# Performance work log

Measured on AMD Instinct MI355X. Metric: run time of the kernel, lower is better.

Reference implementation:

```python
import jax, jax.numpy as jnp
import numpy as np

B, L, DIN = 16, 4096, 1280
DM, N, R, NL = 128, 16, 8, 2  # d_model=d_inner, d_state, dt_rank, num_layers


def setup_inputs() -> dict:
    key = jax.random.key(0)
    ks = jax.random.split(key, 16)
    f = lambda i, shape, s=0.02: jax.random.normal(ks[i], shape, jnp.float32) * s
    return dict(
        x=jax.random.normal(ks[0], (B, L, DIN), jnp.float32),
        ip_w=f(1, (DM, DIN)), ip_b=f(2, (DM,)),
        in_w=f(3, (NL, 2 * DM, DM)),              # in_proj (no bias), out = [x; z]
        conv_w=f(4, (NL, DM, 2), 0.5), conv_b=f(5, (NL, DM)),  # depthwise causal conv, k=2
        xp_w=f(6, (NL, R + 2 * N, DM)),           # x_proj -> [dt; B; C]
        dt_w=f(7, (NL, DM, R), 0.5), dt_b=f(8, (NL, DM)),
        A_log=jnp.broadcast_to(jnp.log(jnp.arange(1, N + 1, dtype=jnp.float32)), (NL, DM, N)),
        Dp=jnp.ones((NL, DM), jnp.float32),
        out_w=f(9, (NL, DM, DM)),
        ln_g=jnp.ones((DM,), jnp.float32), ln_b=jnp.zeros((DM,), jnp.float32),
        c1_w=f(10, (64, DM)), c1_b=f(11, (64,)),
        c2_w=f(12, (2, 64)), c2_b=f(13, (2,)),
    )


def _mamba(x, in_w, conv_w, conv_b, xp_w, dt_w, dt_b, A_log, Dp, out_w):
    # x: [B,L,DM]
    Bsz, Ls, _ = x.shape
    xz = jnp.einsum('bld,ed->ble', x, in_w)          # [B,L,2*DM]
    u, z = jnp.split(xz, 2, axis=-1)                  # each [B,L,DM]
    # causal depthwise conv, kernel size 2: y_t = w0*u_{t-1} + w1*u_t + b
    u_prev = jnp.pad(u, ((0, 0), (1, 0), (0, 0)))[:, :Ls]
    u = jax.nn.silu(u_prev * conv_w[:, 0] + u * conv_w[:, 1] + conv_b)
    proj = jnp.einsum('bld,ed->ble', u, xp_w)         # [B,L,R+2N]
    dt, Bm, Cm = jnp.split(proj, [R, R + N], axis=-1)
    delta = jax.nn.softplus(jnp.einsum('blr,dr->bld', dt, dt_w) + dt_b)  # [B,L,DM]
    A = -jnp.exp(A_log)                               # [DM,N]

    def step(h, inp):
        d_t, b_t, c_t, u_t = inp                      # [B,DM],[B,N],[B,N],[B,DM]
        dA = jnp.exp(d_t[..., None] * A)              # [B,DM,N]
        h = h * dA + (d_t * u_t)[..., None] * b_t[:, None, :]
        y = jnp.einsum('bdn,bn->bd', h, c_t)
        return h, y

    h0 = jnp.zeros((Bsz, DM, N), x.dtype)
    xs = (delta.transpose(1, 0, 2), Bm.transpose(1, 0, 2),
          Cm.transpose(1, 0, 2), u.transpose(1, 0, 2))
    _, ys = jax.lax.scan(step, h0, xs)                # ys: [L,B,DM]
    y = ys.transpose(1, 0, 2) + u * Dp
    y = y * jax.nn.silu(z)
    return jnp.einsum('bld,ed->ble', y, out_w)


def reference(x, ip_w, ip_b, in_w, conv_w, conv_b, xp_w, dt_w, dt_b, A_log, Dp,
              out_w, ln_g, ln_b, c1_w, c1_b, c2_w, c2_b):
    h = jnp.einsum('bli,di->bld', x, ip_w) + ip_b     # input_proj
    for l in range(NL):                               # residual Mamba blocks
        h = h + _mamba(h, in_w[l], conv_w[l], conv_b[l], xp_w[l], dt_w[l],
                       dt_b[l], A_log[l], Dp[l], out_w[l])
    mu = jnp.mean(h, -1, keepdims=True)
    var = jnp.mean((h - mu) ** 2, -1, keepdims=True)
    h = (h - mu) / jnp.sqrt(var + 1e-5) * ln_g + ln_b # LayerNorm
    p = jnp.mean(h, axis=1)                           # mean pool over seq
    p = jax.nn.relu(p @ c1_w.T + c1_b)                # classifier (dropout=eval/no-op)
    return p @ c2_w.T + c2_b                          # [B,2]
```

## Files before the change

### kernel.cpp

```cpp
#include <hip/hip_runtime.h>
#include <hip/hip_bf16.h>
#include <cstdint>

#define B_   16
#define L_   4096
#define DIN_ 1280
#define DM_  128
#define NS_  16
#define RR_  8
#define NL_  2
#define M_   (B_ * L_)
#define NC_  128
#define CL_  (L_ / NC_)

typedef short short8 __attribute__((ext_vector_type(8)));
typedef float f32x4  __attribute__((ext_vector_type(4)));
typedef unsigned short ushort;
typedef ushort ushort4v __attribute__((ext_vector_type(4)));

__device__ __forceinline__ float silu_f(float x) { return x / (1.f + __expf(-x)); }

__device__ __forceinline__ ushort f2bf(float f) {
  union { float f; uint32_t u; } v; v.f = f;
  uint32_t u = v.u;
  u += 0x7fffu + ((u >> 16) & 1u);
  return (ushort)(u >> 16);
}

#define LDK 40

__global__ __launch_bounds__(256) void gemm_mfma(
    const float* __restrict__ A, const float* __restrict__ W,
    const float* __restrict__ bias,
    float* __restrict__ C0, float* __restrict__ C1,
    int M, int Nc, int K, int split, int residual)
{
  __shared__ ushort As[128 * LDK];
  __shared__ ushort Ws[128 * LDK];
  const int tid = threadIdx.x;
  const int n0 = blockIdx.x * 128;
  const int m0 = blockIdx.y * 128;

  const int srow = tid >> 1;
  const int scol = (tid & 1) << 4;
  const float* gA = A + (size_t)(m0 + srow) * K + scol;
  const float* gW = W + (size_t)(n0 + srow) * K + scol;

  const int lane = tid & 63;
  const int wv = tid >> 6;
  const int wm = (wv & 1) * 64, wn = (wv >> 1) * 64;
  const int ln15 = lane & 15, quad = lane >> 4;

  f32x4 acc[4][4];
#pragma unroll
  for (int i = 0; i < 4; ++i)
#pragma unroll
    for (int j = 0; j < 4; ++j) acc[i][j] = (f32x4){0.f, 0.f, 0.f, 0.f};

  float4 fa[4], fw[4];
#pragma unroll
  for (int j = 0; j < 4; ++j) {
    fa[j] = *(const float4*)(gA + j * 4);
    fw[j] = *(const float4*)(gW + j * 4);
  }

  for (int k0 = 0; k0 < K; k0 += 32) {
    __syncthreads();
#pragma unroll
    for (int j = 0; j < 4; ++j) {
      ushort4v a4 = { f2bf(fa[j].x), f2bf(fa[j].y), f2bf(fa[j].z), f2bf(fa[j].w) };
      ushort4v w4 = { f2bf(fw[j].x), f2bf(fw[j].y), f2bf(fw[j].z), f2bf(fw[j].w) };
      *(ushort4v*)&As[srow * LDK + scol + j * 4] = a4;
      *(ushort4v*)&Ws[srow * LDK + scol + j * 4] = w4;
    }
    if (k0 + 32 < K) {
#pragma unroll
      for (int j = 0; j < 4; ++j) {
        fa[j] = *(const float4*)(gA + k0 + 32 + j * 4);
        fw[j] = *(const float4*)(gW + k0 + 32 + j * 4);
      }
    }
    __syncthreads();
    short8 aF[4], bF[4];
#pragma unroll
    for (int mt = 0; mt < 4; ++mt)
      aF[mt] = *(const short8*)&As[(wm + mt * 16 + ln15) * LDK + quad * 8];
#pragma unroll
    for (int nt = 0; nt < 4; ++nt)
      bF[nt] = *(const short8*)&Ws[(wn + nt * 16 + ln15) * LDK + quad * 8];
#pragma unroll
    for (int mt = 0; mt < 4; ++mt)
#pragma unroll
      for (int nt = 0; nt < 4; ++nt)
        acc[mt][nt] = __builtin_amdgcn_mfma_f32_16x16x32_bf16(
            aF[mt], bF[nt], acc[mt][nt], 0, 0, 0);
  }

  const bool left = n0 < split;
#pragma unroll
  for (int mt = 0; mt < 4; ++mt) {
    const int row = m0 + wm + mt * 16 + quad * 4;
#pragma unroll
    for (int nt = 0; nt < 4; ++nt) {
      const int col = n0 + wn + nt * 16 + ln15;
      const float bv = bias ? bias[col] : 0.f;
#pragma unroll
      for (int r = 0; r < 4; ++r) {
        float v = acc[mt][nt][r] + bv;
        if (left) {
          float* p = C0 + (size_t)(row + r) * split + col;
          if (residual) v += *p;
          *p = v;
        } else {
          C1[(size_t)(row + r) * (Nc - split) + (col - split)] = silu_f(v);
        }
      }
    }
  }
}

__global__ __launch_bounds__(256) void xpc(
    const float* __restrict__ uraw,
    const float* __restrict__ cw, const float* __restrict__ cb,
    const float* __restrict__ xpw,
    const float* __restrict__ dtw,
    const float* __restrict__ dtb,
    float* __restrict__ uout,
    float* __restrict__ delta,
    float* __restrict__ BCout)
{
  __shared__ float u_s[32][132];
  __shared__ float xp_s[40 * 128];
  __shared__ float dtw_s[128 * 8];
  __shared__ float dtb_s[128];
  __shared__ float proj_s[32][41];
  const int tid = threadIdx.x;
  const size_t m0 = (size_t)blockIdx.x * 32;
  const int t0 = (int)(m0 & (L_ - 1));

#pragma unroll
  for (int i = 0; i < 16; ++i) {
    int f = tid + i * 256;
    int tok = f >> 7, dd = f & 127;
    float cur = uraw[(m0 + tok) * DM_ + dd];
    float prev = (t0 + tok > 0) ? uraw[(m0 + tok - 1) * DM_ + dd] : 0.f;
    float v = silu_f(cw[dd * 2] * prev + cw[dd * 2 + 1] * cur + cb[dd]);
    u_s[tok][dd] = v;
    uout[(m0 + tok) * DM_ + dd] = v;
  }
  for (int f = tid; f < 40 * 128; f += 256) xp_s[f] = xpw[f];
  for (int f = tid; f < 128 * 8; f += 256) dtw_s[f] = dtw[f];
  if (tid < 128) dtb_s[tid] = dtb[tid];
  __syncthreads();

  {
    const int tok = tid & 31, eg = tid >> 5;
    float pa[5] = {0.f, 0.f, 0.f, 0.f, 0.f};
    for (int dd = 0; dd < 128; dd += 4) {
      float4 uu = *(const float4*)&u_s[tok][dd];
#pragma unroll
      for (int i = 0; i < 5; ++i) {
        float4 xv = *(const float4*)&xp_s[(eg * 5 + i) * 128 + dd];
        pa[i] += uu.x * xv.x + uu.y * xv.y + uu.z * xv.z + uu.w * xv.w;
      }
    }
#pragma unroll
    for (int i = 0; i < 5; ++i) proj_s[tok][eg * 5 + i] = pa[i];
  }
  __syncthreads();

#pragma unroll
  for (int i = 0; i < 4; ++i) {
    int f = tid + i * 256;
    BCout[m0 * 32 + f] = proj_s[f >> 5][8 + (f & 31)];
  }

  {
    const int tok = tid & 31, dg = tid >> 5;
    float pr[8];
#pragma unroll
    for (int r = 0; r < 8; ++r) pr[r] = proj_s[tok][r];
#pragma unroll
    for (int jj = 0; jj < 16; ++jj) {
      int dd = dg * 16 + jj;
      float acc = dtb_s[dd];
#pragma unroll
      for (int r = 0; r < 8; ++r) acc += pr[r] * dtw_s[dd * 8 + r];
      float sp = (acc > 20.f) ? acc : log1pf(__expf(acc));
      u_s[tok][dd] = sp;
    }
  }
  __syncthreads();
#pragma unroll
  for (int i = 0; i < 16; ++i) {
    int f = tid + i * 256;
    delta[(m0 + (f >> 7)) * DM_ + (f & 127)] = u_s[f >> 7][f & 127];
  }
}

__global__ __launch_bounds__(128) void scan_h(
    const float* __restrict__ delta, const float* __restrict__ u,
    const float* __restrict__ BC, const float* __restrict__ alog,
    float* __restrict__ hend, float* __restrict__ Ssum)
{
  const int d = threadIdx.x;
  const int chunk = blockIdx.x, b = blockIdx.y;
  float a[NS_], h[NS_];
#pragma unroll
  for (int n = 0; n < NS_; ++n) {
    a[n] = -__expf(alog[d * NS_ + n]);
    h[n] = 0.f;
  }
  float S = 0.f;
  const size_t rowbase = (size_t)b * L_ + (size_t)chunk * CL_;
  float dlt = delta[rowbase * DM_ + d];
  float uu  = u[rowbase * DM_ + d];
  for (int s = 0; s < CL_; ++s) {
    const float* Brow = BC + (rowbase + s) * 32;
    float Bv[NS_];
#pragma unroll
    for (int n = 0; n < NS_; ++n) Bv[n] = Brow[n];
    float dn = 0.f, un = 0.f;
    if (s + 1 < CL_) {
      dn = delta[(rowbase + s + 1) * DM_ + d];
      un = u[(rowbase + s + 1) * DM_ + d];
    }
    const float du = dlt * uu;
    S += dlt;
#pragma unroll
    for (int n = 0; n < NS_; ++n) {
      float dA = __expf(dlt * a[n]);
      h[n] = fmaf(h[n], dA, du * Bv[n]);
    }
    dlt = dn; uu = un;
  }
  const size_t o = ((size_t)b * NC_ + chunk) * DM_ + d;
  float4* hp = (float4*)(hend + o * NS_);
#pragma unroll
  for (int q = 0; q < 4; ++q)
    hp[q] = make_float4(h[q * 4], h[q * 4 + 1], h[q * 4 + 2], h[q * 4 + 3]);
  Ssum[o] = S;
}

__global__ __launch_bounds__(256) void scan_comb(
    const float* __restrict__ hend, const float* __restrict__ Ssum,
    const float* __restrict__ alog, float* __restrict__ hstart)
{
  const int idx = blockIdx.x * 256 + threadIdx.x;
  const int n = idx & 15;
  const int d = (idx >> 4) & 127;
  const int b = idx >> 11;
  const float a = -__expf(alog[d * NS_ + n]);
  float hs = 0.f;
  for (int c = 0; c < NC_; ++c) {
    const size_t o = ((size_t)b * NC_ + c) * DM_ + d;
    hstart[o * NS_ + n] = hs;
    hs = hend[o * NS_ + n] + __expf(a * Ssum[o]) * hs;
  }
}

__global__ __launch_bounds__(128) void scan_y(
    const float* __restrict__ delta, const float* __restrict__ u,
    const float* __restrict__ zbuf, const float* __restrict__ BC,
    const float* __restrict__ alog, const float* __restrict__ Dpv,
    const float* __restrict__ hstart, float* __restrict__ y)
{
  const int d = threadIdx.x;
  const int chunk = blockIdx.x, b = blockIdx.y;
  float a[NS_], h[NS_];
  const size_t o = ((size_t)b * NC_ + chunk) * DM_ + d;
  const float4* hp = (const float4*)(hstart + o * NS_);
#pragma unroll
  for (int q = 0; q < 4; ++q) {
    float4 v = hp[q];
    h[q * 4] = v.x; h[q * 4 + 1] = v.y; h[q * 4 + 2] = v.z; h[q * 4 + 3] = v.w;
  }
#pragma unroll
  for (int n = 0; n < NS_; ++n) a[n] = -__expf(alog[d * NS_ + n]);
  const float Dd = Dpv[d];
  const size_t rowbase = (size_t)b * L_ + (size_t)chunk * CL_;
  float dlt = delta[rowbase * DM_ + d];
  float uu  = u[rowbase * DM_ + d];
  float zz  = zbuf[rowbase * DM_ + d];
  for (int s = 0; s < CL_; ++s) {
    const float* Brow = BC + (rowbase + s) * 32;
    float Bv[NS_], Cv[NS_];
#pragma unroll
    for (int n = 0; n < NS_; ++n) { Bv[n] = Brow[n]; Cv[n] = Brow[16 + n]; }
    float dn = 0.f, un = 0.f, zn = 0.f;
    if (s + 1 < CL_) {
      dn = delta[(rowbase + s + 1) * DM_ + d];
      un = u[(rowbase + s + 1) * DM_ + d];
      zn = zbuf[(rowbase + s + 1) * DM_ + d];
    }
    const float du = dlt * uu;
    float yv = uu * Dd;
#pragma unroll
    for (int n = 0; n < NS_; ++n) {
      float dA = __expf(dlt * a[n]);
      h[n] = fmaf(h[n], dA, du * Bv[n]);
      yv = fmaf(h[n], Cv[n], yv);
    }
    y[(rowbase + s) * DM_ + d] = yv * zz;
    dlt = dn; uu = un; zz = zn;
  }
}

__global__ __launch_bounds__(256) void lnpool1(
    const float* __restrict__ h, float* __restrict__ partial)
{
  const int b = blockIdx.y, ch = blockIdx.x;
  const int tid = threadIdx.x, wave = tid >> 6, lane = tid & 63;
  float a0 = 0.f, a1 = 0.f;
  const int tbase = ch * 256 + wave * 64;
  for (int i = 0; i < 64; ++i) {
    const float* row = h + ((size_t)b * L_ + tbase + i) * DM_;
    float x0 = row[lane], x1 = row[lane + 64];
    float s = x0 + x1, sq = x0 * x0 + x1 * x1;
    for (int off = 32; off; off >>= 1) { s += __shfl_xor(s, off); sq += __shfl_xor(sq, off); }
    float mu = s * (1.f / 128.f);
    float var = sq * (1.f / 128.f) - mu * mu;
    float rstd = rsqrtf(var + 1e-5f);
    a0 += (x0 - mu) * rstd;
    a1 += (x1 - mu) * rstd;
  }
  __shared__ float ps[4][128];
  ps[wave][lane] = a0;
  ps[wave][lane + 64] = a1;
  __syncthreads();
  if (tid < 128)
    partial[((size_t)b * 16 + ch) * DM_ + tid] = ps[0][tid] + ps[1][tid] + ps[2][tid] + ps[3][tid];
}

__global__ __launch_bounds__(256) void headk(
    const float* __restrict__ partial,
    const float* __restrict__ lng, const float* __restrict__ lnb,
    const float* __restrict__ c1w, const float* __restrict__ c1b,
    const float* __restrict__ c2w, const float* __restrict__ c2b,
    float* __restrict__ out)
{
  __shared__ float pool[16][128];
  __shared__ float p1[16][64];
  const int tid = threadIdx.x;
  for (int i = tid; i < 16 * 128; i += 256) {
    int b = i >> 7, dd = i & 127;
    float s = 0.f;
    for (int c = 0; c < 16; ++c) s += partial[((size_t)b * 16 + c) * DM_ + dd];
    pool[b][dd] = s * (1.f / (float)L_) * lng[dd] + lnb[dd];
  }
  __syncthreads();
  for (int i = tid; i < 16 * 64; i += 256) {
    int b = i >> 6, j = i & 63;
    float acc = c1b[j];
    for (int dd = 0; dd < 128; ++dd) acc += pool[b][dd] * c1w[j * 128 + dd];
    p1[b][j] = fmaxf(acc, 0.f);
  }
  __syncthreads();
  if (tid < 32) {
    int b = tid >> 1, k = tid & 1;
    float acc = c2b[k];
    for (int j = 0; j < 64; ++j) acc += p1[b][j] * c2w[k * 64 + j];
    out[b * 2 + k] = acc;
  }
}

extern "C" void kernel_launch(void* const* d_in, const int* in_sizes, int n_in,
                              void* d_out, int out_size, void* d_ws, size_t ws_size,
                              hipStream_t stream)
{
  (void)in_sizes; (void)n_in; (void)out_size; (void)ws_size;
  const float* x    = (const float*)d_in[0];
  const float* ipw  = (const float*)d_in[1];
  const float* ipb  = (const float*)d_in[2];
  const float* inw  = (const float*)d_in[3];
  const float* cw   = (const float*)d_in[4];
  const float* cb   = (const float*)d_in[5];
  const float* xpw  = (const float*)d_in[6];
  const float* dtw  = (const float*)d_in[7];
  const float* dtb  = (const float*)d_in[8];
  const float* alog = (const float*)d_in[9];
  const float* Dpv  = (const float*)d_in[10];
  const float* outw = (const float*)d_in[11];
  const float* lng  = (const float*)d_in[12];
  const float* lnb  = (const float*)d_in[13];
  const float* c1w  = (const float*)d_in[14];
  const float* c1b  = (const float*)d_in[15];
  const float* c2w  = (const float*)d_in[16];
  const float* c2b  = (const float*)d_in[17];

  float* ws = (float*)d_ws;
  const size_t SZ = (size_t)M_ * DM_;
  float* h      = ws;
  float* yraw   = h + SZ;
  float* zbuf   = yraw + SZ;
  float* ubuf   = zbuf + SZ;
  float* dbuf   = ubuf + SZ;
  float* bc     = dbuf + SZ;
  float* hend   = bc + (size_t)M_ * 32;
  float* hstart = hend + (size_t)B_ * NC_ * DM_ * NS_;
  float* Ssum   = hstart + (size_t)B_ * NC_ * DM_ * NS_;
  float* part   = Ssum + (size_t)B_ * NC_ * DM_;

  gemm_mfma<<<dim3(1, M_ / 128), 256, 0, stream>>>(
      x, ipw, ipb, h, nullptr, M_, DM_, DIN_, DM_, 0);

  for (int l = 0; l < NL_; ++l) {
    gemm_mfma<<<dim3(2, M_ / 128), 256, 0, stream>>>(
        h, inw + (size_t)l * 256 * DM_, nullptr, yraw, zbuf, M_, 256, DM_, DM_, 0);
    xpc<<<M_ / 32, 256, 0, stream>>>(
        yraw, cw + l * DM_ * 2, cb + l * DM_,
        xpw + l * 40 * DM_, dtw + l * DM_ * RR_, dtb + l * DM_,
        ubuf, dbuf, bc);
    scan_h<<<dim3(NC_, B_), 128, 0, stream>>>(
        dbuf, ubuf, bc, alog + l * DM_ * NS_, hend, Ssum);
    scan_comb<<<(B_ * DM_ * NS_) / 256, 256, 0, stream>>>(
        hend, Ssum, alog + l * DM_ * NS_, hstart);
    scan_y<<<dim3(NC_, B_), 128, 0, stream>>>(
        dbuf, ubuf, zbuf, bc, alog + l * DM_ * NS_, Dpv + l * DM_, hstart, yraw);
    gemm_mfma<<<dim3(1, M_ / 128), 256, 0, stream>>>(
        yraw, outw + (size_t)l * DM_ * DM_, nullptr, h, nullptr, M_, DM_, DM_, DM_, 1);
  }

  lnpool1<<<dim3(16, B_), 256, 0, stream>>>(h, part);
  headk<<<1, 256, 0, stream>>>(part, lng, lnb, c1w, c1b, c2w, c2b, (float*)d_out);
}
```

Baseline: 914.1 us.

## Store intermediate activations in bf16 and stage BC rows in shared memory

Intermediate buffers (u, z, delta, B/C projections, y) now hold bf16 instead of fp32, and weights are converted to bf16 once by a small kernel so the GEMMs load half the bytes. The scan kernels stage each chunk's B/C rows into shared memory once rather than re-reading them from global memory at every step, and the chunk-combine loop prefetches the next chunk's values. The aim is to cut memory traffic across the whole pipeline. The cost is lower precision in the delta and state inputs to the recurrence, plus three extra conversion launches per call.

```diff
diff --git a/kernel.cpp b/kernel.cpp
--- a/kernel.cpp
+++ b/kernel.cpp
@@ -17,6 +17,7 @@
 typedef float f32x4  __attribute__((ext_vector_type(4)));
 typedef unsigned short ushort;
 typedef ushort ushort4v __attribute__((ext_vector_type(4)));
+typedef ushort ushort8v __attribute__((ext_vector_type(8)));
 
 __device__ __forceinline__ float silu_f(float x) { return x / (1.f + __expf(-x)); }
 
@@ -26,25 +27,40 @@
   u += 0x7fffu + ((u >> 16) & 1u);
   return (ushort)(u >> 16);
 }
+__device__ __forceinline__ float bf2f(ushort h) {
+  union { uint32_t u; float f; } v; v.u = ((uint32_t)h) << 16; return v.f;
+}
+
+__global__ __launch_bounds__(256) void wcvt(
+    const float* __restrict__ src, ushort* __restrict__ dst, int n)
+{
+  int i = (blockIdx.x * 256 + threadIdx.x) * 4;
+  if (i < n) {
+    float4 v = *(const float4*)(src + i);
+    ushort4v o = { f2bf(v.x), f2bf(v.y), f2bf(v.z), f2bf(v.w) };
+    *(ushort4v*)(dst + i) = o;
+  }
+}
 
 #define LDK 40
 
-__global__ __launch_bounds__(256) void gemm_mfma(
-    const float* __restrict__ A, const float* __restrict__ W,
-    const float* __restrict__ bias,
-    float* __restrict__ C0, float* __restrict__ C1,
-    int M, int Nc, int K, int split, int residual)
+__global__ __launch_bounds__(256) void gemm_bf(
+    const float* __restrict__ Af, const ushort* __restrict__ Ab,
+    const ushort* __restrict__ Wb, const float* __restrict__ bias,
+    float* __restrict__ C0f, ushort* __restrict__ C0b, ushort* __restrict__ C1b,
+    int Ncols, int K, int split, int residual)
 {
   __shared__ ushort As[128 * LDK];
   __shared__ ushort Ws[128 * LDK];
   const int tid = threadIdx.x;
   const int n0 = blockIdx.x * 128;
   const int m0 = blockIdx.y * 128;
-
   const int srow = tid >> 1;
   const int scol = (tid & 1) << 4;
-  const float* gA = A + (size_t)(m0 + srow) * K + scol;
-  const float* gW = W + (size_t)(n0 + srow) * K + scol;
+  const bool abf = (Ab != nullptr);
+  const float*  gAf = Af + (size_t)(m0 + srow) * K + scol;
+  const ushort* gAb = Ab + (size_t)(m0 + srow) * K + scol;
+  const ushort* gW  = Wb + (size_t)(n0 + srow) * K + scol;
 
   const int lane = tid & 63;
   const int wv = tid >> 6;
@@ -57,28 +73,39 @@
 #pragma unroll
     for (int j = 0; j < 4; ++j) acc[i][j] = (f32x4){0.f, 0.f, 0.f, 0.f};
 
-  float4 fa[4], fw[4];
-#pragma unroll
-  for (int j = 0; j < 4; ++j) {
-    fa[j] = *(const float4*)(gA + j * 4);
-    fw[j] = *(const float4*)(gW + j * 4);
-  }
+  float4 fa[4];
+  ushort8v ba0, ba1, bw0, bw1;
+  if (abf) { ba0 = *(const ushort8v*)gAb; ba1 = *(const ushort8v*)(gAb + 8); }
+  else {
+#pragma unroll
+    for (int j = 0; j < 4; ++j) fa[j] = *(const float4*)(gAf + j * 4);
+  }
+  bw0 = *(const ushort8v*)gW; bw1 = *(const ushort8v*)(gW + 8);
 
   for (int k0 = 0; k0 < K; k0 += 32) {
     __syncthreads();
-#pragma unroll
-    for (int j = 0; j < 4; ++j) {
-      ushort4v a4 = { f2bf(fa[j].x), f2bf(fa[j].y), f2bf(fa[j].z), f2bf(fa[j].w) };
-      ushort4v w4 = { f2bf(fw[j].x), f2bf(fw[j].y), f2bf(fw[j].z), f2bf(fw[j].w) };
-      *(ushort4v*)&As[srow * LDK + scol + j * 4] = a4;
-      *(ushort4v*)&Ws[srow * LDK + scol + j * 4] = w4;
-    }
+    if (abf) {
+      *(ushort8v*)&As[srow * LDK + scol]     = ba0;
+      *(ushort8v*)&As[srow * LDK + scol + 8] = ba1;
+    } else {
+#pragma unroll
+      for (int j = 0; j < 4; ++j) {
+        ushort4v a4 = { f2bf(fa[j].x), f2bf(fa[j].y), f2bf(fa[j].z), f2bf(fa[j].w) };
+        *(ushort4v*)&As[srow * LDK + scol + j * 4] = a4;
+      }
+    }
+    *(ushort8v*)&Ws[srow * LDK + scol]     = bw0;
+    *(ushort8v*)&Ws[srow * LDK + scol + 8] = bw1;
     if (k0 + 32 < K) {
-#pragma unroll
-      for (int j = 0; j < 4; ++j) {
-        fa[j] = *(const float4*)(gA + k0 + 32 + j * 4);
-        fw[j] = *(const float4*)(gW + k0 + 32 + j * 4);
+      if (abf) {
+        ba0 = *(const ushort8v*)(gAb + k0 + 32);
+        ba1 = *(const ushort8v*)(gAb + k0 + 40);
+      } else {
+#pragma unroll
+        for (int j = 0; j < 4; ++j) fa[j] = *(const float4*)(gAf + k0 + 32 + j * 4);
       }
+      bw0 = *(const ushort8v*)(gW + k0 + 32);
+      bw1 = *(const ushort8v*)(gW + k0 + 40);
     }
     __syncthreads();
     short8 aF[4], bF[4];
@@ -107,12 +134,17 @@
 #pragma unroll
       for (int r = 0; r < 4; ++r) {
         float v = acc[mt][nt][r] + bv;
+        const int rr = row + r;
         if (left) {
-          float* p = C0 + (size_t)(row + r) * split + col;
-          if (residual) v += *p;
-          *p = v;
+          if (C0f) {
+            float* p = C0f + (size_t)rr * split + col;
+            if (residual) v += *p;
+            *p = v;
+          } else {
+            C0b[(size_t)rr * split + col] = f2bf(v);
+          }
         } else {
-          C1[(size_t)(row + r) * (Nc - split) + (col - split)] = silu_f(v);
+          C1b[(size_t)rr * (Ncols - split) + (col - split)] = f2bf(silu_f(v));
         }
       }
     }
@@ -120,14 +152,14 @@
 }
 
 __global__ __launch_bounds__(256) void xpc(
-    const float* __restrict__ uraw,
+    const ushort* __restrict__ uraw,
     const float* __restrict__ cw, const float* __restrict__ cb,
     const float* __restrict__ xpw,
     const float* __restrict__ dtw,
     const float* __restrict__ dtb,
-    float* __restrict__ uout,
-    float* __restrict__ delta,
-    float* __restrict__ BCout)
+    ushort* __restrict__ uout,
+    ushort* __restrict__ delta,
+    ushort* __restrict__ bcout)
 {
   __shared__ float u_s[32][132];
   __shared__ float xp_s[40 * 128];
@@ -142,11 +174,11 @@
   for (int i = 0; i < 16; ++i) {
     int f = tid + i * 256;
     int tok = f >> 7, dd = f & 127;
-    float cur = uraw[(m0 + tok) * DM_ + dd];
-    float prev = (t0 + tok > 0) ? uraw[(m0 + tok - 1) * DM_ + dd] : 0.f;
+    float cur = bf2f(uraw[(m0 + tok) * DM_ + dd]);
+    float prev = (t0 + tok > 0) ? bf2f(uraw[(m0 + tok - 1) * DM_ + dd]) : 0.f;
     float v = silu_f(cw[dd * 2] * prev + cw[dd * 2 + 1] * cur + cb[dd]);
     u_s[tok][dd] = v;
-    uout[(m0 + tok) * DM_ + dd] = v;
+    uout[(m0 + tok) * DM_ + dd] = f2bf(v);
   }
   for (int f = tid; f < 40 * 128; f += 256) xp_s[f] = xpw[f];
   for (int f = tid; f < 128 * 8; f += 256) dtw_s[f] = dtw[f];
@@ -172,7 +204,7 @@
 #pragma unroll
   for (int i = 0; i < 4; ++i) {
     int f = tid + i * 256;
-    BCout[m0 * 32 + f] = proj_s[f >> 5][8 + (f & 31)];
+    bcout[m0 * 32 + f] = f2bf(proj_s[f >> 5][8 + (f & 31)]);
   }
 
   {
@@ -194,17 +226,25 @@
 #pragma unroll
   for (int i = 0; i < 16; ++i) {
     int f = tid + i * 256;
-    delta[(m0 + (f >> 7)) * DM_ + (f & 127)] = u_s[f >> 7][f & 127];
+    delta[(m0 + (f >> 7)) * DM_ + (f & 127)] = f2bf(u_s[f >> 7][f & 127]);
   }
 }
 
 __global__ __launch_bounds__(128) void scan_h(
-    const float* __restrict__ delta, const float* __restrict__ u,
-    const float* __restrict__ BC, const float* __restrict__ alog,
+    const ushort* __restrict__ delta, const ushort* __restrict__ u,
+    const ushort* __restrict__ BCb, const float* __restrict__ alog,
     float* __restrict__ hend, float* __restrict__ Ssum)
 {
+  __shared__ float bcs[CL_][32];
   const int d = threadIdx.x;
   const int chunk = blockIdx.x, b = blockIdx.y;
+  const size_t rowbase = (size_t)b * L_ + (size_t)chunk * CL_;
+  {
+    ushort8v v = *(const ushort8v*)(BCb + rowbase * 32 + (size_t)d * 8);
+    float* dst = &bcs[0][0] + d * 8;
+#pragma unroll
+    for (int j = 0; j < 8; ++j) dst[j] = bf2f(v[j]);
+  }
   float a[NS_], h[NS_];
 #pragma unroll
   for (int n = 0; n < NS_; ++n) {
@@ -212,19 +252,19 @@
     h[n] = 0.f;
   }
   float S = 0.f;
-  const size_t rowbase = (size_t)b * L_ + (size_t)chunk * CL_;
-  float dlt = delta[rowbase * DM_ + d];
-  float uu  = u[rowbase * DM_ + d];
+  __syncthreads();
+  float dlt = bf2f(delta[rowbase * DM_ + d]);
+  float uu  = bf2f(u[rowbase * DM_ + d]);
   for (int s = 0; s < CL_; ++s) {
-    const float* Brow = BC + (rowbase + s) * 32;
-    float Bv[NS_];
-#pragma unroll
-    for (int n = 0; n < NS_; ++n) Bv[n] = Brow[n];
     float dn = 0.f, un = 0.f;
     if (s + 1 < CL_) {
-      dn = delta[(rowbase + s + 1) * DM_ + d];
-      un = u[(rowbase + s + 1) * DM_ + d];
-    }
+      dn = bf2f(delta[(rowbase + s + 1) * DM_ + d]);
+      un = bf2f(u[(rowbase + s + 1) * DM_ + d]);
+    }
+    float Bv[NS_];
+#pragma unroll
+    for (int q = 0; q < 4; ++q)
+      *(float4*)&Bv[q * 4] = *(const float4*)&bcs[s][q * 4];
     const float du = dlt * uu;
     S += dlt;
 #pragma unroll
@@ -252,21 +292,34 @@
   const int b = idx >> 11;
   const float a = -__expf(alog[d * NS_ + n]);
   float hs = 0.f;
+  size_t o = (size_t)b * NC_ * DM_ + d;
+  float he = hend[o * NS_ + n], ss = Ssum[o];
   for (int c = 0; c < NC_; ++c) {
-    const size_t o = ((size_t)b * NC_ + c) * DM_ + d;
+    const size_t on = o + DM_;
+    float hen = 0.f, ssn = 0.f;
+    if (c + 1 < NC_) { hen = hend[on * NS_ + n]; ssn = Ssum[on]; }
     hstart[o * NS_ + n] = hs;
-    hs = hend[o * NS_ + n] + __expf(a * Ssum[o]) * hs;
+    hs = he + __expf(a * ss) * hs;
+    he = hen; ss = ssn; o = on;
   }
 }
 
 __global__ __launch_bounds__(128) void scan_y(
-    const float* __restrict__ delta, const float* __restrict__ u,
-    const float* __restrict__ zbuf, const float* __restrict__ BC,
+    const ushort* __restrict__ delta, const ushort* __restrict__ u,
+    const ushort* __restrict__ zb, const ushort* __restrict__ BCb,
     const float* __restrict__ alog, const float* __restrict__ Dpv,
-    const float* __restrict__ hstart, float* __restrict__ y)
-{
+    const float* __restrict__ hstart, ushort* __restrict__ y)
+{
+  __shared__ float bcs[CL_][32];
   const int d = threadIdx.x;
   const int chunk = blockIdx.x, b = blockIdx.y;
+  const size_t rowbase = (size_t)b * L_ + (size_t)chunk * CL_;
+  {
+    ushort8v v = *(const ushort8v*)(BCb + rowbase * 32 + (size_t)d * 8);
+    float* dst = &bcs[0][0] + d * 8;
+#pragma unroll
+    for (int j = 0; j < 8; ++j) dst[j] = bf2f(v[j]);
+  }
   float a[NS_], h[NS_];
   const size_t o = ((size_t)b * NC_ + chunk) * DM_ + d;
   const float4* hp = (const float4*)(hstart + o * NS_);
@@ -278,20 +331,22 @@
 #pragma unroll
   for (int n = 0; n < NS_; ++n) a[n] = -__expf(alog[d * NS_ + n]);
   const float Dd = Dpv[d];
-  const size_t rowbase = (size_t)b * L_ + (size_t)chunk * CL_;
-  float dlt = delta[rowbase * DM_ + d];
-  float uu  = u[rowbase * DM_ + d];
-  float zz  = zbuf[rowbase * DM_ + d];
+  __syncthreads();
+  float dlt = bf2f(delta[rowbase * DM_ + d]);
+  float uu  = bf2f(u[rowbase * DM_ + d]);
+  float zz  = bf2f(zb[rowbase * DM_ + d]);
   for (int s = 0; s < CL_; ++s) {
-    const float* Brow = BC + (rowbase + s) * 32;
-    float Bv[NS_], Cv[NS_];
-#pragma unroll
-    for (int n = 0; n < NS_; ++n) { Bv[n] = Brow[n]; Cv[n] = Brow[16 + n]; }
     float dn = 0.f, un = 0.f, zn = 0.f;
     if (s + 1 < CL_) {
-      dn = delta[(rowbase + s + 1) * DM_ + d];
-      un = u[(rowbase + s + 1) * DM_ + d];
-      zn = zbuf[(rowbase + s + 1) * DM_ + d];
+      dn = bf2f(delta[(rowbase + s + 1) * DM_ + d]);
+      un = bf2f(u[(rowbase + s + 1) * DM_ + d]);
+      zn = bf2f(zb[(rowbase + s + 1) * DM_ + d]);
+    }
+    float Bv[NS_], Cv[NS_];
+#pragma unroll
+    for (int q = 0; q < 4; ++q) {
+      *(float4*)&Bv[q * 4] = *(const float4*)&bcs[s][q * 4];
+      *(float4*)&Cv[q * 4] = *(const float4*)&bcs[s][16 + q * 4];
     }
     const float du = dlt * uu;
     float yv = uu * Dd;
@@ -301,7 +356,7 @@
       h[n] = fmaf(h[n], dA, du * Bv[n]);
       yv = fmaf(h[n], Cv[n], yv);
     }
-    y[(rowbase + s) * DM_ + d] = yv * zz;
+    y[(rowbase + s) * DM_ + d] = f2bf(yv * zz);
     dlt = dn; uu = un; zz = zn;
   }
 }
@@ -391,34 +446,45 @@
   float* ws = (float*)d_ws;
   const size_t SZ = (size_t)M_ * DM_;
   float* h      = ws;
-  float* yraw   = h + SZ;
-  float* zbuf   = yraw + SZ;
-  float* ubuf   = zbuf + SZ;
-  float* dbuf   = ubuf + SZ;
-  float* bc     = dbuf + SZ;
-  float* hend   = bc + (size_t)M_ * 32;
+  float* hend   = h + SZ;
   float* hstart = hend + (size_t)B_ * NC_ * DM_ * NS_;
   float* Ssum   = hstart + (size_t)B_ * NC_ * DM_ * NS_;
   float* part   = Ssum + (size_t)B_ * NC_ * DM_;
-
-  gemm_mfma<<<dim3(1, M_ / 128), 256, 0, stream>>>(
-      x, ipw, ipb, h, nullptr, M_, DM_, DIN_, DM_, 0);
+  ushort* bfb   = (ushort*)(part + (size_t)B_ * 16 * DM_);
+  ushort* urawb = bfb;
+  ushort* ub    = urawb + SZ;
+  ushort* zbuf  = ub + SZ;
+  ushort* dbuf  = zbuf + SZ;
+  ushort* ybuf  = dbuf + SZ;
+  ushort* bcb   = ybuf + SZ;
+  ushort* wipb  = bcb + (size_t)M_ * 32;
+  ushort* winb  = wipb + (size_t)DM_ * DIN_;
+  ushort* woutb = winb + (size_t)NL_ * 2 * DM_ * DM_;
+
+  wcvt<<<(DM_ * DIN_ / 4 + 255) / 256, 256, 0, stream>>>(ipw, wipb, DM_ * DIN_);
+  wcvt<<<(NL_ * 2 * DM_ * DM_ / 4 + 255) / 256, 256, 0, stream>>>(inw, winb, NL_ * 2 * DM_ * DM_);
+  wcvt<<<(NL_ * DM_ * DM_ / 4 + 255) / 256, 256, 0, stream>>>(outw, woutb, NL_ * DM_ * DM_);
+
+  gemm_bf<<<dim3(1, M_ / 128), 256, 0, stream>>>(
+      x, nullptr, wipb, ipb, h, nullptr, nullptr, DM_, DIN_, DM_, 0);
 
   for (int l = 0; l < NL_; ++l) {
-    gemm_mfma<<<dim3(2, M_ / 128), 256, 0, stream>>>(
-        h, inw + (size_t)l * 256 * DM_, nullptr, yraw, zbuf, M_, 256, DM_, DM_, 0);
+    gemm_bf<<<dim3(2, M_ / 128), 256, 0, stream>>>(
+        h, nullptr, winb + (size_t)l * 2 * DM_ * DM_, nullptr,
+        nullptr, urawb, zbuf, 2 * DM_, DM_, DM_, 0);
     xpc<<<M_ / 32, 256, 0, stream>>>(
-        yraw, cw + l * DM_ * 2, cb + l * DM_,
-        xpw + l * 40 * DM_, dtw + l * DM_ * RR_, dtb + l * DM_,
-        ubuf, dbuf, bc);
+        urawb, cw + l * DM_ * 2, cb + l * DM_,
+        xpw + l * (RR_ + 2 * NS_) * DM_, dtw + l * DM_ * RR_, dtb + l * DM_,
+        ub, dbuf, bcb);
     scan_h<<<dim3(NC_, B_), 128, 0, stream>>>(
-        dbuf, ubuf, bc, alog + l * DM_ * NS_, hend, Ssum);
+        dbuf, ub, bcb, alog + l * DM_ * NS_, hend, Ssum);
     scan_comb<<<(B_ * DM_ * NS_) / 256, 256, 0, stream>>>(
         hend, Ssum, alog + l * DM_ * NS_, hstart);
     scan_y<<<dim3(NC_, B_), 128, 0, stream>>>(
-        dbuf, ubuf, zbuf, bc, alog + l * DM_ * NS_, Dpv + l * DM_, hstart, yraw);
-    gemm_mfma<<<dim3(1, M_ / 128), 256, 0, stream>>>(
-        yraw, outw + (size_t)l * DM_ * DM_, nullptr, h, nullptr, M_, DM_, DM_, DM_, 1);
+        dbuf, ub, zbuf, bcb, alog + l * DM_ * NS_, Dpv + l * DM_, hstart, ybuf);
+    gemm_bf<<<dim3(1, M_ / 128), 256, 0, stream>>>(
+        nullptr, ybuf, woutb + (size_t)l * DM_ * DM_, nullptr,
+        h, nullptr, nullptr, DM_, DM_, DM_, 1);
   }
 
   lnpool1<<<dim3(16, B_), 256, 0, stream>>>(h, part);
```

Result: no change. 926.7 us (+1.4%).
